# Optimization experiments

Measured on AMD Instinct MI355X. Metric: run time of the kernel, lower is better.

## Reference

```python
import jax, jax.numpy as jnp
import numpy as np

N_NODES = 100000
N_EDGES = 3200000
IN_FEAT = 128
OUT_FEAT = 128
NUM_RELS = 16
NUM_BASES = 8


def setup_inputs() -> dict:
    key = jax.random.key(0)
    ks = jax.random.split(key, 7)
    x = jax.random.normal(ks[0], (N_NODES, IN_FEAT), dtype=jnp.float32)
    src = jax.random.randint(ks[1], (N_EDGES,), 0, N_NODES, dtype=jnp.int64)
    dst = jax.random.randint(ks[2], (N_EDGES,), 0, N_NODES, dtype=jnp.int64)
    etypes = jax.random.randint(ks[3], (N_EDGES,), 0, NUM_RELS, dtype=jnp.int64)
    # xavier_uniform with gain for relu = sqrt(2)
    gain = float(np.sqrt(2.0))
    limit_w = gain * float(np.sqrt(6.0 / (IN_FEAT + OUT_FEAT)))
    weight = jax.random.uniform(ks[4], (NUM_BASES, IN_FEAT, OUT_FEAT), dtype=jnp.float32,
                                minval=-limit_w, maxval=limit_w)
    limit_c = float(np.sqrt(6.0 / (NUM_RELS + NUM_BASES)))
    w_comp = jax.random.uniform(ks[5], (NUM_RELS, NUM_BASES), dtype=jnp.float32,
                                minval=-limit_c, maxval=limit_c)
    h_bias = jnp.zeros((OUT_FEAT,), dtype=jnp.float32)
    return {"x": x, "weight": weight, "w_comp": w_comp, "h_bias": h_bias,
            "src": src, "dst": dst, "etypes": etypes}


def reference(x, weight, w_comp, h_bias, src, dst, etypes):
    # basis decomposition: per-relation weight [R, in, out]
    W = jnp.einsum('rb,bio->rio', w_comp, weight)
    # transform all nodes under every relation: h[r, n, o]
    h = jnp.einsum('ni,rio->rno', x, W)
    # per-edge message = transformed source feature under the edge's relation type
    msg = h[etypes, src]  # [E, out]
    # scatter-sum messages into destination nodes
    node_repr = jax.ops.segment_sum(msg, dst, num_segments=N_NODES)
    node_repr = node_repr + h_bias
    return node_repr
```

## Files before the change

kernel.cpp:

```cpp
#include <hip/hip_runtime.h>
#include <hip/hip_bf16.h>
#include <stdint.h>

#define N_NODES   100000
#define N_EDGES   3200000
#define IN_FEAT   128
#define OUT_FEAT  128
#define NUM_RELS  16
#define NUM_BASES 8
#define M_PAD     100096
#define NBKT      391
#define NB        512

using short8 = __attribute__((ext_vector_type(8))) short;
using v4f    = __attribute__((ext_vector_type(4))) float;

__device__ inline unsigned short f2bf_rne(float f) {
    __hip_bfloat16 h = __float2bfloat16(f);
    return *reinterpret_cast<unsigned short*>(&h);
}
__device__ inline float bf2f(unsigned short u) {
    union { uint32_t i; float f; } x;
    x.i = ((uint32_t)u) << 16;
    return x.f;
}

__global__ void conv_x(const float* __restrict__ x, unsigned short* __restrict__ xb) {
    int id = blockIdx.x * 256 + threadIdx.x;
    int base = id * 4;
    ushort4 o;
    if (base < N_NODES * IN_FEAT) {
        const float4 v = reinterpret_cast<const float4*>(x)[id];
        o.x = f2bf_rne(v.x); o.y = f2bf_rne(v.y);
        o.z = f2bf_rne(v.z); o.w = f2bf_rne(v.w);
    } else {
        o.x = o.y = o.z = o.w = 0;
    }
    reinterpret_cast<ushort4*>(xb)[id] = o;
}

__global__ void build_ut(const float* __restrict__ weight,
                         unsigned short* __restrict__ Ut) {
    int id = blockIdx.x * 256 + threadIdx.x;
    int o  = id >> 10;
    int kk = id & 1023;
    int b  = kk >> 7;
    int i  = kk & 127;
    Ut[id] = f2bf_rne(weight[(b * IN_FEAT + i) * OUT_FEAT + o]);
}

__global__ __launch_bounds__(512) void coarse_hist(const int* __restrict__ dst,
                                                   int* __restrict__ histG,
                                                   int nbuck) {
    extern __shared__ int lh[];
    for (int i = threadIdx.x; i < nbuck; i += 512) lh[i] = 0;
    __syncthreads();
    const int NG = N_EDGES / 4;
    const int stride = NB * 512;
    for (int g = blockIdx.x * 512 + threadIdx.x; g < NG; g += stride) {
        const int4 d4 = reinterpret_cast<const int4*>(dst)[g];
        atomicAdd(&lh[d4.x >> 8], 1);
        atomicAdd(&lh[d4.y >> 8], 1);
        atomicAdd(&lh[d4.z >> 8], 1);
        atomicAdd(&lh[d4.w >> 8], 1);
    }
    __syncthreads();
    for (int i = threadIdx.x; i < nbuck; i += 512)
        histG[i * NB + blockIdx.x] = lh[i];
}

__global__ void scan_part(const int* __restrict__ data, int* __restrict__ partial, int K) {
    __shared__ int sh[256];
    const int tid = threadIdx.x, b = blockIdx.x;
    const int i0 = b * 4096 + tid * 16;
    int s = 0;
#pragma unroll
    for (int k = 0; k < 16; ++k) { int i = i0 + k; if (i < K) s += data[i]; }
    sh[tid] = s;
    __syncthreads();
    for (int st = 128; st > 0; st >>= 1) {
        if (tid < st) sh[tid] += sh[tid + st];
        __syncthreads();
    }
    if (tid == 0) partial[b] = sh[0];
}

__global__ __launch_bounds__(512) void scan_mid(int* __restrict__ partial, int G) {
    __shared__ int sh[512];
    const int tid = threadIdx.x;
    int v = (tid < G) ? partial[tid] : 0;
    sh[tid] = v;
    __syncthreads();
    for (int st = 1; st < 512; st <<= 1) {
        int t = (tid >= st) ? sh[tid - st] : 0;
        __syncthreads();
        sh[tid] += t;
        __syncthreads();
    }
    if (tid < G) partial[tid] = sh[tid] - v;
}

__global__ void scan_final(int* __restrict__ data, const int* __restrict__ partial, int K) {
    __shared__ int sh[256];
    const int tid = threadIdx.x, b = blockIdx.x;
    const int i0 = b * 4096 + tid * 16;
    int s = 0;
#pragma unroll
    for (int k = 0; k < 16; ++k) { int i = i0 + k; if (i < K) s += data[i]; }
    sh[tid] = s;
    __syncthreads();
    for (int st = 1; st < 256; st <<= 1) {
        int t = (tid >= st) ? sh[tid - st] : 0;
        __syncthreads();
        sh[tid] += t;
        __syncthreads();
    }
    int run = partial[b] + sh[tid] - s;
#pragma unroll
    for (int k = 0; k < 16; ++k) {
        int i = i0 + k;
        if (i < K) {
            int c = data[i];
            data[i] = run;
            run += c;
        }
    }
}

__global__ __launch_bounds__(512) void coarse_place(const int* __restrict__ src,
                                                    const int* __restrict__ dst,
                                                    const int* __restrict__ et,
                                                    const int* __restrict__ histS,
                                                    int* __restrict__ entries,
                                                    int nbuck) {
    extern __shared__ int cur[];
    for (int i = threadIdx.x; i < nbuck; i += 512)
        cur[i] = histS[i * NB + blockIdx.x];
    __syncthreads();
    const int NG = N_EDGES / 4;
    const int stride = NB * 512;
    for (int g = blockIdx.x * 512 + threadIdx.x; g < NG; g += stride) {
        const int4 s4 = reinterpret_cast<const int4*>(src)[g];
        const int4 d4 = reinterpret_cast<const int4*>(dst)[g];
        const int4 t4 = reinterpret_cast<const int4*>(et)[g];
        int p0 = atomicAdd(&cur[d4.x >> 8], 1);
        int p1 = atomicAdd(&cur[d4.y >> 8], 1);
        int p2 = atomicAdd(&cur[d4.z >> 8], 1);
        int p3 = atomicAdd(&cur[d4.w >> 8], 1);
        entries[p0] = ((d4.x & 255) << 21) | (s4.x << 4) | (t4.x & 15);
        entries[p1] = ((d4.y & 255) << 21) | (s4.y << 4) | (t4.y & 15);
        entries[p2] = ((d4.z & 255) << 21) | (s4.z << 4) | (t4.z & 15);
        entries[p3] = ((d4.w & 255) << 21) | (s4.w << 4) | (t4.w & 15);
    }
}

__global__ __launch_bounds__(256) void fine_sort(const int* __restrict__ entries,
                                                 const int* __restrict__ histS,
                                                 int* __restrict__ perm,
                                                 int* __restrict__ off,
                                                 int nbuck) {
    __shared__ int cnt[256];
    __shared__ int bs[256];
    const int tid = threadIdx.x, b = blockIdx.x;
    const int start = histS[b * NB];
    const int end   = (b + 1 < nbuck) ? histS[(b + 1) * NB] : N_EDGES;

    cnt[tid] = 0;
    __syncthreads();
    for (int i = start + tid; i < end; i += 256)
        atomicAdd(&cnt[entries[i] >> 21], 1);
    __syncthreads();

    int v = cnt[tid];
    bs[tid] = v;
    __syncthreads();
    for (int st = 1; st < 256; st <<= 1) {
        int t = (tid >= st) ? bs[tid - st] : 0;
        __syncthreads();
        bs[tid] += t;
        __syncthreads();
    }
    const int excl = bs[tid] - v;

    const int d = b * 256 + tid;
    if (d < N_NODES) off[d] = start + excl;
    if (b == nbuck - 1 && tid == 0) off[N_NODES] = N_EDGES;

    __syncthreads();
    cnt[tid] = excl;
    __syncthreads();
    for (int i = start + tid; i < end; i += 256) {
        int en = entries[i];
        int p = atomicAdd(&cnt[en >> 21], 1);
        perm[start + p] = en & 0x1FFFFF;
    }
}

__global__ void gather_z(const int* __restrict__ off, const int* __restrict__ perm,
                         const unsigned short* __restrict__ xb,
                         const float* __restrict__ w_comp,
                         unsigned short* __restrict__ zb) {
    __shared__ float csh[NUM_RELS * NUM_BASES];
    if (threadIdx.x < NUM_RELS * NUM_BASES) csh[threadIdx.x] = w_comp[threadIdx.x];
    __syncthreads();
    const int d = blockIdx.x * 4 + (threadIdx.x >> 6);
    const int lane = threadIdx.x & 63;
    float2 z[8];
#pragma unroll
    for (int b = 0; b < 8; ++b) z[b] = make_float2(0.f, 0.f);
    if (d < N_NODES) {
        const int e0 = off[d], e1 = off[d + 1];
        const unsigned short* xl = xb + lane * 2;
        int e = e0;
        for (; e + 8 <= e1; e += 8) {
            int p[8];
#pragma unroll
            for (int j = 0; j < 8; ++j) p[j] = perm[e + j];
            ushort2 v[8];
#pragma unroll
            for (int j = 0; j < 8; ++j)
                v[j] = *reinterpret_cast<const ushort2*>(xl + (size_t)(p[j] >> 4) * 128);
#pragma unroll
            for (int j = 0; j < 8; ++j) {
                const float4 cA = *reinterpret_cast<const float4*>(&csh[(p[j] & 15) * 8]);
                const float4 cB = *reinterpret_cast<const float4*>(&csh[(p[j] & 15) * 8 + 4]);
                const float xlo = bf2f(v[j].x), xhi = bf2f(v[j].y);
                z[0].x += cA.x * xlo; z[0].y += cA.x * xhi;
                z[1].x += cA.y * xlo; z[1].y += cA.y * xhi;
                z[2].x += cA.z * xlo; z[2].y += cA.z * xhi;
                z[3].x += cA.w * xlo; z[3].y += cA.w * xhi;
                z[4].x += cB.x * xlo; z[4].y += cB.x * xhi;
                z[5].x += cB.y * xlo; z[5].y += cB.y * xhi;
                z[6].x += cB.z * xlo; z[6].y += cB.z * xhi;
                z[7].x += cB.w * xlo; z[7].y += cB.w * xhi;
            }
        }
        for (; e < e1; ++e) {
            int p = perm[e];
            ushort2 v = *reinterpret_cast<const ushort2*>(xl + (size_t)(p >> 4) * 128);
            const float4 cA = *reinterpret_cast<const float4*>(&csh[(p & 15) * 8]);
            const float4 cB = *reinterpret_cast<const float4*>(&csh[(p & 15) * 8 + 4]);
            const float xlo = bf2f(v.x), xhi = bf2f(v.y);
            z[0].x += cA.x * xlo; z[0].y += cA.x * xhi;
            z[1].x += cA.y * xlo; z[1].y += cA.y * xhi;
            z[2].x += cA.z * xlo; z[2].y += cA.z * xhi;
            z[3].x += cA.w * xlo; z[3].y += cA.w * xhi;
            z[4].x += cB.x * xlo; z[4].y += cB.x * xhi;
            z[5].x += cB.y * xlo; z[5].y += cB.y * xhi;
            z[6].x += cB.z * xlo; z[6].y += cB.z * xhi;
            z[7].x += cB.w * xlo; z[7].y += cB.w * xhi;
        }
    }
    unsigned short* zr = zb + (size_t)d * 1024 + lane * 2;
#pragma unroll
    for (int b = 0; b < 8; ++b) {
        ushort2 o;
        o.x = f2bf_rne(z[b].x);
        o.y = f2bf_rne(z[b].y);
        *reinterpret_cast<ushort2*>(zr + b * 128) = o;
    }
}

__global__ __launch_bounds__(256, 2) void zgemm(const unsigned short* __restrict__ zb,
                                                const unsigned short* __restrict__ Ut,
                                                const float* __restrict__ bias,
                                                float* __restrict__ out) {
    __shared__ unsigned short lA[128 * 128];
    __shared__ unsigned short lB[128 * 128];

    const int mb = blockIdx.x;
    const int tid  = threadIdx.x;
    const int wid  = tid >> 6;
    const int lane = tid & 63;
    const int wm = wid >> 1, wn = wid & 1;
    const int ml = lane & 15, kgrp = lane >> 4;

    const unsigned short* gA = zb + (size_t)mb * 128 * 1024;

    v4f acc[4][4];
#pragma unroll
    for (int i = 0; i < 4; ++i)
#pragma unroll
        for (int j = 0; j < 4; ++j)
            acc[i][j] = (v4f){0.f, 0.f, 0.f, 0.f};

    for (int kt = 0; kt < 8; ++kt) {
#pragma unroll
        for (int it = 0; it < 8; ++it) {
            int sbase = it * 256 + wid * 64;
            int s = sbase + lane;
            int row = s >> 4;
            int cc = (s & 15) ^ (row & 15);
            __builtin_amdgcn_global_load_lds(
                (const __attribute__((address_space(1))) void*)(gA + (size_t)row * 1024 + kt * 128 + cc * 8),
                (__attribute__((address_space(3))) void*)(&lA[sbase * 8]), 16, 0, 0);
            __builtin_amdgcn_global_load_lds(
                (const __attribute__((address_space(1))) void*)(Ut + (size_t)row * 1024 + kt * 128 + cc * 8),
                (__attribute__((address_space(3))) void*)(&lB[sbase * 8]), 16, 0, 0);
        }
        __syncthreads();

#pragma unroll
        for (int kb = 0; kb < 4; ++kb) {
            const int cc = kb * 4 + kgrp;
            short8 af[4], bfr[4];
#pragma unroll
            for (int tm = 0; tm < 4; ++tm) {
                int rA = wm * 64 + tm * 16 + ml;
                af[tm] = *reinterpret_cast<const short8*>(&lA[(rA * 16 + (cc ^ (rA & 15))) * 8]);
            }
#pragma unroll
            for (int tn = 0; tn < 4; ++tn) {
                int rB = wn * 64 + tn * 16 + ml;
                bfr[tn] = *reinterpret_cast<const short8*>(&lB[(rB * 16 + (cc ^ (rB & 15))) * 8]);
            }
#pragma unroll
            for (int tm = 0; tm < 4; ++tm)
#pragma unroll
                for (int tn = 0; tn < 4; ++tn)
                    acc[tm][tn] = __builtin_amdgcn_mfma_f32_16x16x32_bf16(af[tm], bfr[tn], acc[tm][tn], 0, 0, 0);
        }
        __syncthreads();
    }

    const int row0 = mb * 128 + wm * 64;
    const int col0 = wn * 64;
#pragma unroll
    for (int tm = 0; tm < 4; ++tm)
#pragma unroll
        for (int rr = 0; rr < 4; ++rr) {
            int row = row0 + tm * 16 + kgrp * 4 + rr;
            if (row < N_NODES) {
                size_t rb = (size_t)row * OUT_FEAT;
#pragma unroll
                for (int tn = 0; tn < 4; ++tn) {
                    int col = col0 + tn * 16 + ml;
                    out[rb + col] = acc[tm][tn][rr] + bias[col];
                }
            }
        }
}

static inline size_t align256(size_t a) { return (a + 255) & ~(size_t)255; }

extern "C" void kernel_launch(void* const* d_in, const int* in_sizes, int n_in,
                              void* d_out, int out_size, void* d_ws, size_t ws_size,
                              hipStream_t stream) {
    const float* x      = (const float*)d_in[0];
    const float* weight = (const float*)d_in[1];
    const float* w_comp = (const float*)d_in[2];
    const float* h_bias = (const float*)d_in[3];
    const int*   src    = (const int*)d_in[4];
    const int*   dst    = (const int*)d_in[5];
    const int*   etypes = (const int*)d_in[6];
    float* out = (float*)d_out;

    const int nbuck = NBKT;
    const int K2 = nbuck * NB;
    const int G2 = (K2 + 4095) / 4096;

    size_t a = 512 * 1024;
    size_t xb_o = a;   a = align256(a + (size_t)M_PAD * 128 * 2);
    size_t perm_o = a; a = align256(a + (size_t)N_EDGES * 4);
    size_t off_o = a;  a = align256(a + ((size_t)N_NODES + 1) * 4);
    size_t part_o = a; a = align256(a + 512 * 4);
    size_t zb_o = a;

    char* w = (char*)d_ws;
    unsigned short* Ut      = (unsigned short*)(w);
    unsigned short* xb      = (unsigned short*)(w + xb_o);
    int*            perm    = (int*)(w + perm_o);
    int*            off     = (int*)(w + off_o);
    int*            partial = (int*)(w + part_o);
    unsigned short* zb      = (unsigned short*)(w + zb_o);
    int*            entries = (int*)(w + zb_o);
    int*            histG   = (int*)(w + zb_o + 13 * 1024 * 1024);

    conv_x<<<12512, 256, 0, stream>>>(x, xb);
    build_ut<<<512, 256, 0, stream>>>(weight, Ut);

    coarse_hist<<<NB, 512, nbuck * 4, stream>>>(dst, histG, nbuck);
    scan_part<<<G2, 256, 0, stream>>>(histG, partial, K2);
    scan_mid<<<1, 512, 0, stream>>>(partial, G2);
    scan_final<<<G2, 256, 0, stream>>>(histG, partial, K2);
    coarse_place<<<NB, 512, nbuck * 4, stream>>>(src, dst, etypes, histG, entries, nbuck);
    fine_sort<<<nbuck, 256, 0, stream>>>(entries, histG, perm, off, nbuck);

    gather_z<<<25024, 256, 0, stream>>>(off, perm, xb, w_comp, zb);
    zgemm<<<782, 256, 0, stream>>>(zb, Ut, h_bias, out);
}
```

Before: 424.6 us.

## Sort edges by destination then relation to batch per-relation basis coefficients

Repacks edge entries so the relation type sits above the source index, and the fine sort now buckets on (dst, relation) with 4096 counters per block. Edges of a node are then grouped by relation. The gather kernel sums raw x features within each run of equal relation and applies the 8 basis coefficients once per run rather than once per edge, which removes most of the per-edge FMAs and LDS coefficient reads. It also writes z with a packed nontemporal store. In exchange, the sort uses a larger LDS histogram, each thread does a 16-wide serial scan, and the gather has a data-dependent branch that can diverge across lanes.

```diff
diff --git a/kernel.cpp b/kernel.cpp
--- a/kernel.cpp
+++ b/kernel.cpp
@@ -147,10 +147,10 @@
         int p1 = atomicAdd(&cur[d4.y >> 8], 1);
         int p2 = atomicAdd(&cur[d4.z >> 8], 1);
         int p3 = atomicAdd(&cur[d4.w >> 8], 1);
-        entries[p0] = ((d4.x & 255) << 21) | (s4.x << 4) | (t4.x & 15);
-        entries[p1] = ((d4.y & 255) << 21) | (s4.y << 4) | (t4.y & 15);
-        entries[p2] = ((d4.z & 255) << 21) | (s4.z << 4) | (t4.z & 15);
-        entries[p3] = ((d4.w & 255) << 21) | (s4.w << 4) | (t4.w & 15);
+        entries[p0] = ((d4.x & 255) << 21) | ((t4.x & 15) << 17) | s4.x;
+        entries[p1] = ((d4.y & 255) << 21) | ((t4.y & 15) << 17) | s4.y;
+        entries[p2] = ((d4.z & 255) << 21) | ((t4.z & 15) << 17) | s4.z;
+        entries[p3] = ((d4.w & 255) << 21) | ((t4.w & 15) << 17) | s4.w;
     }
 }
 
@@ -159,20 +159,24 @@
                                                  int* __restrict__ perm,
                                                  int* __restrict__ off,
                                                  int nbuck) {
-    __shared__ int cnt[256];
+    __shared__ int cnt[4096];
     __shared__ int bs[256];
     const int tid = threadIdx.x, b = blockIdx.x;
     const int start = histS[b * NB];
     const int end   = (b + 1 < nbuck) ? histS[(b + 1) * NB] : N_EDGES;
 
-    cnt[tid] = 0;
+#pragma unroll
+    for (int k = 0; k < 16; ++k) cnt[tid * 16 + k] = 0;
     __syncthreads();
     for (int i = start + tid; i < end; i += 256)
-        atomicAdd(&cnt[entries[i] >> 21], 1);
-    __syncthreads();
-
-    int v = cnt[tid];
-    bs[tid] = v;
+        atomicAdd(&cnt[entries[i] >> 17], 1);
+    __syncthreads();
+
+    int c[16];
+    int tsum = 0;
+#pragma unroll
+    for (int k = 0; k < 16; ++k) { c[k] = cnt[tid * 16 + k]; tsum += c[k]; }
+    bs[tid] = tsum;
     __syncthreads();
     for (int st = 1; st < 256; st <<= 1) {
         int t = (tid >= st) ? bs[tid - st] : 0;
@@ -180,18 +184,19 @@
         bs[tid] += t;
         __syncthreads();
     }
-    const int excl = bs[tid] - v;
+    const int excl = bs[tid] - tsum;
 
     const int d = b * 256 + tid;
     if (d < N_NODES) off[d] = start + excl;
     if (b == nbuck - 1 && tid == 0) off[N_NODES] = N_EDGES;
 
-    __syncthreads();
-    cnt[tid] = excl;
+    int run = excl;
+#pragma unroll
+    for (int k = 0; k < 16; ++k) { cnt[tid * 16 + k] = run; run += c[k]; }
     __syncthreads();
     for (int i = start + tid; i < end; i += 256) {
         int en = entries[i];
-        int p = atomicAdd(&cnt[en >> 21], 1);
+        int p = atomicAdd(&cnt[en >> 17], 1);
         perm[start + p] = en & 0x1FFFFF;
     }
 }
@@ -208,56 +213,67 @@
     float2 z[8];
 #pragma unroll
     for (int b = 0; b < 8; ++b) z[b] = make_float2(0.f, 0.f);
+
     if (d < N_NODES) {
         const int e0 = off[d], e1 = off[d + 1];
         const unsigned short* xl = xb + lane * 2;
-        int e = e0;
-        for (; e + 8 <= e1; e += 8) {
-            int p[8];
-#pragma unroll
-            for (int j = 0; j < 8; ++j) p[j] = perm[e + j];
-            ushort2 v[8];
-#pragma unroll
-            for (int j = 0; j < 8; ++j)
-                v[j] = *reinterpret_cast<const ushort2*>(xl + (size_t)(p[j] >> 4) * 128);
-#pragma unroll
-            for (int j = 0; j < 8; ++j) {
-                const float4 cA = *reinterpret_cast<const float4*>(&csh[(p[j] & 15) * 8]);
-                const float4 cB = *reinterpret_cast<const float4*>(&csh[(p[j] & 15) * 8 + 4]);
-                const float xlo = bf2f(v[j].x), xhi = bf2f(v[j].y);
-                z[0].x += cA.x * xlo; z[0].y += cA.x * xhi;
-                z[1].x += cA.y * xlo; z[1].y += cA.y * xhi;
-                z[2].x += cA.z * xlo; z[2].y += cA.z * xhi;
-                z[3].x += cA.w * xlo; z[3].y += cA.w * xhi;
-                z[4].x += cB.x * xlo; z[4].y += cB.x * xhi;
-                z[5].x += cB.y * xlo; z[5].y += cB.y * xhi;
-                z[6].x += cB.z * xlo; z[6].y += cB.z * xhi;
-                z[7].x += cB.w * xlo; z[7].y += cB.w * xhi;
-            }
+        int cur = -1;
+        float2 srun = make_float2(0.f, 0.f);
+
+        auto flush = [&]() {
+            const float4 cA = *reinterpret_cast<const float4*>(&csh[cur * 8]);
+            const float4 cB = *reinterpret_cast<const float4*>(&csh[cur * 8 + 4]);
+            z[0].x += cA.x * srun.x; z[0].y += cA.x * srun.y;
+            z[1].x += cA.y * srun.x; z[1].y += cA.y * srun.y;
+            z[2].x += cA.z * srun.x; z[2].y += cA.z * srun.y;
+            z[3].x += cA.w * srun.x; z[3].y += cA.w * srun.y;
+            z[4].x += cB.x * srun.x; z[4].y += cB.x * srun.y;
+            z[5].x += cB.y * srun.x; z[5].y += cB.y * srun.y;
+            z[6].x += cB.z * srun.x; z[6].y += cB.z * srun.y;
+            z[7].x += cB.w * srun.x; z[7].y += cB.w * srun.y;
+        };
+        auto step = [&](int p, ushort2 v) {
+            int rl = p >> 17;
+            if (rl != cur) {
+                flush();
+                cur = rl;
+                srun = make_float2(0.f, 0.f);
+            }
+            srun.x += bf2f(v.x);
+            srun.y += bf2f(v.y);
+        };
+
+        if (e0 < e1) {
+            cur = perm[e0] >> 17;
+            int e = e0;
+            for (; e + 8 <= e1; e += 8) {
+                int p[8];
+#pragma unroll
+                for (int j = 0; j < 8; ++j) p[j] = perm[e + j];
+                ushort2 v[8];
+#pragma unroll
+                for (int j = 0; j < 8; ++j)
+                    v[j] = *reinterpret_cast<const ushort2*>(
+                        xl + (size_t)(p[j] & 0x1FFFF) * 128);
+#pragma unroll
+                for (int j = 0; j < 8; ++j) step(p[j], v[j]);
+            }
+            for (; e < e1; ++e) {
+                int p = perm[e];
+                ushort2 v = *reinterpret_cast<const ushort2*>(
+                    xl + (size_t)(p & 0x1FFFF) * 128);
+                step(p, v);
+            }
+            flush();
         }
-        for (; e < e1; ++e) {
-            int p = perm[e];
-            ushort2 v = *reinterpret_cast<const ushort2*>(xl + (size_t)(p >> 4) * 128);
-            const float4 cA = *reinterpret_cast<const float4*>(&csh[(p & 15) * 8]);
-            const float4 cB = *reinterpret_cast<const float4*>(&csh[(p & 15) * 8 + 4]);
-            const float xlo = bf2f(v.x), xhi = bf2f(v.y);
-            z[0].x += cA.x * xlo; z[0].y += cA.x * xhi;
-            z[1].x += cA.y * xlo; z[1].y += cA.y * xhi;
-            z[2].x += cA.z * xlo; z[2].y += cA.z * xhi;
-            z[3].x += cA.w * xlo; z[3].y += cA.w * xhi;
-            z[4].x += cB.x * xlo; z[4].y += cB.x * xhi;
-            z[5].x += cB.y * xlo; z[5].y += cB.y * xhi;
-            z[6].x += cB.z * xlo; z[6].y += cB.z * xhi;
-            z[7].x += cB.w * xlo; z[7].y += cB.w * xhi;
-        }
-    }
+    }
+
     unsigned short* zr = zb + (size_t)d * 1024 + lane * 2;
 #pragma unroll
     for (int b = 0; b < 8; ++b) {
-        ushort2 o;
-        o.x = f2bf_rne(z[b].x);
-        o.y = f2bf_rne(z[b].y);
-        *reinterpret_cast<ushort2*>(zr + b * 128) = o;
+        unsigned int u = (unsigned int)f2bf_rne(z[b].x)
+                       | ((unsigned int)f2bf_rne(z[b].y) << 16);
+        __builtin_nontemporal_store(u, reinterpret_cast<unsigned int*>(zr + b * 128));
     }
 }
 
```

New measurement: 415.3 us. 2.2% less time.
